# Performance work log

Hardware: AMD Instinct MI355X
Metric: run time of the kernel (lower is better)

The kernel has to match this reference:

```python
import jax, jax.numpy as jnp
import numpy as np

N_NODES = 50000
N_EDGES = 800000
DIM = 512
N_CLASSES = 1000


def _xavier(key, shape):
    fan_in, fan_out = shape[0], shape[1]
    lim = float(np.sqrt(6.0 / (fan_in + fan_out)))
    return jax.random.uniform(key, shape, jnp.float32, -lim, lim)


def setup_inputs() -> dict:
    key = jax.random.key(0)
    ks = jax.random.split(key, 12)
    nodes = jax.random.normal(ks[0], (N_NODES, DIM), jnp.float32)
    edges = jax.random.randint(ks[1], (2, N_EDGES), 0, N_NODES, jnp.int64)
    labelmatrix = jax.random.normal(ks[2], (N_CLASSES, 128), jnp.float32)
    return {
        "nodes": nodes,
        "edges": edges,
        "labelmatrix": labelmatrix,
        "W1": _xavier(ks[3], (DIM, 256)), "b1": jnp.zeros((256,), jnp.float32),
        "W2": _xavier(ks[4], (256, 192)), "b2": jnp.zeros((192,), jnp.float32),
        "W3": _xavier(ks[5], (192, 128)), "b3": jnp.zeros((128,), jnp.float32),
        "fc1_w": _xavier(ks[6], (128, 128)), "fc1_b": jnp.zeros((128,), jnp.float32),
        "fc2_w": _xavier(ks[7], (128, 128)), "fc2_b": jnp.zeros((128,), jnp.float32),
    }


def _gcn_conv(x, W, b, src, dst, n):
    # PyG GCNConv: add self-loops, symmetric normalization, then aggregate.
    xw = x @ W                                        # [N, out]
    ones = jnp.ones(src.shape[0], x.dtype)
    deg = jax.ops.segment_sum(ones, dst, num_segments=n) + 1.0  # +1 self-loop
    dinv = jax.lax.rsqrt(deg)                         # deg^{-1/2}
    coef = dinv[src] * dinv[dst]                      # [E]
    agg = jax.ops.segment_sum(xw[src] * coef[:, None], dst, num_segments=n)
    agg = agg + xw * (dinv * dinv)[:, None]           # self-loop contribution
    return agg + b


def reference(nodes, edges, labelmatrix, W1, b1, W2, b2, W3, b3,
              fc1_w, fc1_b, fc2_w, fc2_b):
    src, dst = edges[0], edges[1]
    n = nodes.shape[0]
    # _GraphConv: three stacked GCNConv layers, no inter-layer activation
    x = _gcn_conv(nodes, W1, b1, src, dst, n)
    x = _gcn_conv(x, W2, b2, src, dst, n)
    x = _gcn_conv(x, W3, b3, src, dst, n)             # [N, 128]
    # _GraphLinear (eval mode: dropout is identity)
    h = jax.nn.relu(x @ fc1_w + fc1_b)
    h = h @ fc2_w + fc2_b                             # [N, 128]
    preds = h @ labelmatrix.T                         # dot-product similarity [N, C]
    return preds
```

## Files before the change

### kernel.cpp

```cpp
#include <hip/hip_runtime.h>

typedef unsigned short u16;
typedef __bf16 bf16x8 __attribute__((ext_vector_type(8)));
typedef float f32x4 __attribute__((ext_vector_type(4)));

__device__ __forceinline__ u16 f2bf(float f) {
    unsigned int u = __float_as_uint(f);
    unsigned int r = (u + 0x7FFFu + ((u >> 16) & 1u)) >> 16;
    return (u16)r;
}
__device__ __forceinline__ float bf_lo(unsigned int u) { return __uint_as_float(u << 16); }
__device__ __forceinline__ float bf_hi(unsigned int u) { return __uint_as_float(u & 0xFFFF0000u); }

#define GLOAD_LDS(gp, lp) \
    __builtin_amdgcn_global_load_lds( \
        (const __attribute__((address_space(1))) unsigned int*)(gp), \
        (__attribute__((address_space(3))) unsigned int*)(lp), 16, 0, 0)


__global__ void hist_k(const int* __restrict__ dst, int* __restrict__ deg, int nE) {
    int e = blockIdx.x * 256 + threadIdx.x;
    if (e < nE) atomicAdd(&deg[dst[e]], 1);
}

__global__ void scan_block_k(const int* __restrict__ deg, int* __restrict__ scanned,
                             int* __restrict__ bsums, int n) {
    __shared__ int s[1024];
    int i = blockIdx.x * 1024 + threadIdx.x;
    int v = (i < n) ? deg[i] : 0;
    s[threadIdx.x] = v;
    __syncthreads();
    for (int off = 1; off < 1024; off <<= 1) {
        int t = (threadIdx.x >= off) ? s[threadIdx.x - off] : 0;
        __syncthreads();
        s[threadIdx.x] += t;
        __syncthreads();
    }
    if (i < n) scanned[i] = s[threadIdx.x];
    if (threadIdx.x == 1023) bsums[blockIdx.x] = s[1023];
}

__global__ void scan_sums_k(int* __restrict__ bsums, int nb) {
    int l = threadIdx.x & 63;
    int v = (l < nb) ? bsums[l] : 0;
    int orig = v;
    for (int off = 1; off < 64; off <<= 1) {
        int t = __shfl_up(v, off);
        if (l >= off) v += t;
    }
    if (l < nb) bsums[l] = v - orig;
}

__global__ void scan_final_dinv_k(const int* __restrict__ scanned, const int* __restrict__ deg,
                                  const int* __restrict__ bsums, int* __restrict__ rowptr,
                                  int* __restrict__ wptr, float* __restrict__ dinv,
                                  int n, int nE) {
    int i = blockIdx.x * 256 + threadIdx.x;
    if (i < n) {
        int rp = scanned[i] - deg[i] + bsums[i >> 10];
        rowptr[i] = rp;
        wptr[i] = rp;
        dinv[i] = rsqrtf((float)deg[i] + 1.0f);
    }
    if (i == 0) rowptr[n] = nE;
}

__global__ void csr_fill_k(const int* __restrict__ src, const int* __restrict__ dst,
                           int* __restrict__ wptr, const float* __restrict__ dinv,
                           int* __restrict__ eidx, float* __restrict__ ecoef, int nE) {
    int e = blockIdx.x * 256 + threadIdx.x;
    if (e >= nE) return;
    int d = dst[e], s = src[e];
    int p = atomicAdd(&wptr[d], 1);
    eidx[p] = s;
    ecoef[p] = dinv[s] * dinv[d];
}

__global__ void uv1_k(const int* __restrict__ rowptr, const float* __restrict__ ecoef,
                      const float* __restrict__ dinv, float* __restrict__ u1, int n) {
    int i = blockIdx.x * 256 + threadIdx.x;
    if (i >= n) return;
    float s = dinv[i] * dinv[i];
    int b = rowptr[i], e = rowptr[i + 1];
    for (int k = b; k < e; ++k) s += ecoef[k];
    u1[i] = s;
}

__global__ void uv2_k(const int* __restrict__ rowptr, const int* __restrict__ eidx,
                      const float* __restrict__ ecoef, const float* __restrict__ dinv,
                      const float* __restrict__ u1, float* __restrict__ u2, int n) {
    int i = blockIdx.x * 256 + threadIdx.x;
    if (i >= n) return;
    float s = dinv[i] * dinv[i] * u1[i];
    int b = rowptr[i], e = rowptr[i + 1];
    for (int k = b; k < e; ++k) s += ecoef[k] * u1[eidx[k]];
    u2[i] = s;
}


__global__ __launch_bounds__(192) void ck1_k(const float* __restrict__ W1,
                                             const float* __restrict__ W2,
                                             float* __restrict__ T1) {
    __shared__ float row[256];
    int i = blockIdx.x;
    for (int t = threadIdx.x; t < 256; t += 192) row[t] = W1[i * 256 + t];
    __syncthreads();
    int j = threadIdx.x;
    float s = 0.f;
    for (int k = 0; k < 256; ++k) s = fmaf(row[k], W2[k * 192 + j], s);
    T1[i * 192 + j] = s;
}

__global__ __launch_bounds__(256) void prep2_k(
    const float* __restrict__ T1, const float* __restrict__ W3, u16* __restrict__ Wp,
    const float* __restrict__ b1, const float* __restrict__ W2, const float* __restrict__ b2,
    float* __restrict__ c1, float* __restrict__ c2,
    const float* __restrict__ fc1_w, u16* __restrict__ Bfc1) {
    __shared__ float sbuf[192];
    const int b = blockIdx.x, tid = threadIdx.x;
    if (b < 512) {
        if (tid < 192) sbuf[tid] = T1[b * 192 + tid];
        __syncthreads();
        if (tid < 128) {
            float s = 0.f;
            for (int m = 0; m < 192; ++m) s = fmaf(sbuf[m], W3[m * 128 + tid], s);
            Wp[(size_t)tid * 512 + b] = f2bf(s);
        }
    } else if (b == 512) {
        if (tid < 192) {
            float s = 0.f;
            for (int k = 0; k < 256; ++k) s = fmaf(b1[k], W2[k * 192 + tid], s);
            sbuf[tid] = s;
        }
        __syncthreads();
        if (tid < 128) {
            float a = 0.f, bb = 0.f;
            for (int m = 0; m < 192; ++m) {
                a  = fmaf(sbuf[m], W3[m * 128 + tid], a);
                bb = fmaf(b2[m],   W3[m * 128 + tid], bb);
            }
            c1[tid] = a; c2[tid] = bb;
        }
    } else {
        int idx = (b - 513) * 256 + tid;
        if (idx < 128 * 128) {
            int nn = idx >> 7, k = idx & 127;
            Bfc1[idx] = f2bf(fc1_w[k * 128 + nn]);
        }
    }
}

__global__ __launch_bounds__(128) void fuse_fc2_k(
    const float* __restrict__ fc2_w, const float* __restrict__ fc2_b,
    const float* __restrict__ labelm, u16* __restrict__ Wc, float* __restrict__ bc) {
    __shared__ float w[128 * 129];
    __shared__ float lm[128];
    __shared__ float red[2];
    const int tid = threadIdx.x;
    for (int t = tid; t < 128 * 128; t += 128)
        w[(t >> 7) * 129 + (t & 127)] = fc2_w[t];
    __syncthreads();
    for (int cc = 0; cc < 8; ++cc) {
        int c = blockIdx.x * 8 + cc;
        lm[tid] = (c < 1000) ? labelm[(size_t)c * 128 + tid] : 0.f;
        __syncthreads();
        float sum = 0.f;
        const float* wr = &w[tid * 129];
        for (int j = 0; j < 128; ++j) sum = fmaf(wr[j], lm[j], sum);
        Wc[(size_t)c * 128 + tid] = f2bf(sum);
        float p = fc2_b[tid] * lm[tid];
        for (int off = 32; off > 0; off >>= 1) p += __shfl_down(p, off);
        if ((tid & 63) == 0) red[tid >> 6] = p;
        __syncthreads();
        if (tid == 0) bc[c] = red[0] + red[1];
        __syncthreads();
    }
}


template <bool CASTA, bool OUTF32, bool BIAS, bool RELU>
__global__ __launch_bounds__(256) void gemm_mfma(
    const void* __restrict__ Ap, const u16* __restrict__ Bt,
    const float* __restrict__ bias, void* __restrict__ Cout,
    int K, int Nout, int ldc, int Mout, int lgny, int Arows) {
    __shared__ __align__(16) u16 As[128 * 64];
    __shared__ __align__(16) u16 Bs[128 * 64];
    const int tid  = threadIdx.x;
    const int lane = tid & 63;
    const int w    = tid >> 6;
    const int wm   = w >> 1, wn = w & 1;

    const int nwg = gridDim.x, orig = blockIdx.x;
    const int q = nwg >> 3, r = nwg & 7;
    const int xcd = orig & 7, off = orig >> 3;
    const int tile = (xcd < r ? xcd * (q + 1) : r * (q + 1) + (xcd - r) * q) + off;
    const int ny = 1 << lgny;
    const int tx = tile >> lgny, ty = tile & (ny - 1);
    const size_t bm = (size_t)tx * 128;
    const size_t bn = (size_t)ty * 128;

    const int l7 = lane & 7;
    const int l3 = lane >> 3;
    const int kcs = l7 ^ l3;

    f32x4 acc[4][4] = {};

    for (int k0 = 0; k0 < K; k0 += 64) {
        if constexpr (CASTA) {
            const float* Af = (const float*)Ap;
            const int row = tid >> 1;
            const int half = tid & 1;
            const size_t grow = bm + row;
            const bool valid = grow < (size_t)Arows;
            const float4* g4 = (const float4*)(Af + grow * K + k0 + half * 32);
            float4 f[8];
#pragma unroll
            for (int j = 0; j < 8; ++j)
                f[j] = valid ? g4[j] : make_float4(0.f, 0.f, 0.f, 0.f);
#pragma unroll
            for (int j = 0; j < 4; ++j) {
                int kc = (half * 4 + j) ^ (row & 7);
                uint4 o;
                o.x = (unsigned)f2bf(f[2 * j].x)     | ((unsigned)f2bf(f[2 * j].y) << 16);
                o.y = (unsigned)f2bf(f[2 * j].z)     | ((unsigned)f2bf(f[2 * j].w) << 16);
                o.z = (unsigned)f2bf(f[2 * j + 1].x) | ((unsigned)f2bf(f[2 * j + 1].y) << 16);
                o.w = (unsigned)f2bf(f[2 * j + 1].z) | ((unsigned)f2bf(f[2 * j + 1].w) << 16);
                *(uint4*)((char*)As + row * 128 + kc * 16) = o;
            }
#pragma unroll
            for (int it = 0; it < 4; ++it) {
                const int r0 = w * 32 + it * 8;
                const u16* gB = Bt + ((size_t)(bn + r0 + l3) * K + k0) + kcs * 8;
                GLOAD_LDS(gB, Bs + r0 * 64);
            }
        } else {
            const u16* A = (const u16*)Ap;
#pragma unroll
            for (int it = 0; it < 4; ++it) {
                const int r0 = w * 32 + it * 8;
                const u16* gA = A + ((size_t)(bm + r0 + l3) * K + k0) + kcs * 8;
                GLOAD_LDS(gA, As + r0 * 64);
                const u16* gB = Bt + ((size_t)(bn + r0 + l3) * K + k0) + kcs * 8;
                GLOAD_LDS(gB, Bs + r0 * 64);
            }
        }
        __syncthreads();

#pragma unroll
        for (int ks = 0; ks < 2; ++ks) {
            bf16x8 av[4], bv[4];
#pragma unroll
            for (int i = 0; i < 4; ++i) {
                int row = wm * 64 + i * 16 + (lane & 15);
                int kc = (ks * 4 + (lane >> 4)) ^ (lane & 7);
                av[i] = *(const bf16x8*)((const char*)As + row * 128 + kc * 16);
            }
#pragma unroll
            for (int j = 0; j < 4; ++j) {
                int nn = wn * 64 + j * 16 + (lane & 15);
                int kc = (ks * 4 + (lane >> 4)) ^ (lane & 7);
                bv[j] = *(const bf16x8*)((const char*)Bs + nn * 128 + kc * 16);
            }
#pragma unroll
            for (int i = 0; i < 4; ++i)
#pragma unroll
                for (int j = 0; j < 4; ++j)
                    acc[i][j] = __builtin_amdgcn_mfma_f32_16x16x32_bf16(av[i], bv[j], acc[i][j], 0, 0, 0);
        }
        __syncthreads();
    }

    const int ccol  = lane & 15;
    const int crow4 = (lane >> 4) * 4;
#pragma unroll
    for (int i = 0; i < 4; ++i) {
#pragma unroll
        for (int j = 0; j < 4; ++j) {
#pragma unroll
            for (int r2 = 0; r2 < 4; ++r2) {
                size_t gr = bm + wm * 64 + i * 16 + crow4 + r2;
                size_t gc = bn + wn * 64 + j * 16 + ccol;
                if (gr < (size_t)Mout && gc < (size_t)Nout) {
                    float v = acc[i][j][r2];
                    if constexpr (BIAS) v += bias[gc];
                    if constexpr (RELU) v = fmaxf(v, 0.f);
                    if constexpr (OUTF32) ((float*)Cout)[gr * ldc + gc] = v;
                    else                  ((u16*)Cout)[gr * ldc + gc] = f2bf(v);
                }
            }
        }
    }
}


template <bool FINAL>
__global__ __launch_bounds__(256) void agg128_k(
    const u16* __restrict__ xw, const int* __restrict__ rowptr,
    const int* __restrict__ eidx, const float* __restrict__ ecoef,
    const float* __restrict__ dinv, u16* __restrict__ out,
    const float* __restrict__ u1v, const float* __restrict__ u2v,
    const float* __restrict__ c1, const float* __restrict__ c2,
    const float* __restrict__ b3, int n) {
    const int tid = threadIdx.x;
    const int sub = tid >> 4;
    const int fl  = tid & 15;
    int node = blockIdx.x * 16 + sub;
    if (node >= n) return;

    const uint4* xv = (const uint4*)xw;
    float di = dinv[node];
    float s = di * di;
    uint4 a = xv[(size_t)node * 16 + fl];
    float acc[8];
    acc[0] = s * bf_lo(a.x); acc[1] = s * bf_hi(a.x);
    acc[2] = s * bf_lo(a.y); acc[3] = s * bf_hi(a.y);
    acc[4] = s * bf_lo(a.z); acc[5] = s * bf_hi(a.z);
    acc[6] = s * bf_lo(a.w); acc[7] = s * bf_hi(a.w);

    const int beg = rowptr[node], end = rowptr[node + 1];
    int e = beg;
    for (; e + 7 < end; e += 8) {
        int sn[8]; float cf[8]; uint4 v[8];
#pragma unroll
        for (int q = 0; q < 8; ++q) { sn[q] = eidx[e + q]; cf[q] = ecoef[e + q]; }
#pragma unroll
        for (int q = 0; q < 8; ++q) v[q] = xv[(size_t)sn[q] * 16 + fl];
#pragma unroll
        for (int q = 0; q < 8; ++q) {
            acc[0] = fmaf(cf[q], bf_lo(v[q].x), acc[0]); acc[1] = fmaf(cf[q], bf_hi(v[q].x), acc[1]);
            acc[2] = fmaf(cf[q], bf_lo(v[q].y), acc[2]); acc[3] = fmaf(cf[q], bf_hi(v[q].y), acc[3]);
            acc[4] = fmaf(cf[q], bf_lo(v[q].z), acc[4]); acc[5] = fmaf(cf[q], bf_hi(v[q].z), acc[5]);
            acc[6] = fmaf(cf[q], bf_lo(v[q].w), acc[6]); acc[7] = fmaf(cf[q], bf_hi(v[q].w), acc[7]);
        }
    }
    for (; e < end; ++e) {
        int sn = eidx[e];
        float c = ecoef[e];
        uint4 v = xv[(size_t)sn * 16 + fl];
        acc[0] = fmaf(c, bf_lo(v.x), acc[0]); acc[1] = fmaf(c, bf_hi(v.x), acc[1]);
        acc[2] = fmaf(c, bf_lo(v.y), acc[2]); acc[3] = fmaf(c, bf_hi(v.y), acc[3]);
        acc[4] = fmaf(c, bf_lo(v.z), acc[4]); acc[5] = fmaf(c, bf_hi(v.z), acc[5]);
        acc[6] = fmaf(c, bf_lo(v.w), acc[6]); acc[7] = fmaf(c, bf_hi(v.w), acc[7]);
    }

    if constexpr (FINAL) {
        float uu1 = u1v[node], uu2 = u2v[node];
        float4 c1a = ((const float4*)c1)[fl * 2], c1b = ((const float4*)c1)[fl * 2 + 1];
        float4 c2a = ((const float4*)c2)[fl * 2], c2b = ((const float4*)c2)[fl * 2 + 1];
        float4 b3a = ((const float4*)b3)[fl * 2], b3b = ((const float4*)b3)[fl * 2 + 1];
        acc[0] += uu2 * c1a.x + uu1 * c2a.x + b3a.x;
        acc[1] += uu2 * c1a.y + uu1 * c2a.y + b3a.y;
        acc[2] += uu2 * c1a.z + uu1 * c2a.z + b3a.z;
        acc[3] += uu2 * c1a.w + uu1 * c2a.w + b3a.w;
        acc[4] += uu2 * c1b.x + uu1 * c2b.x + b3b.x;
        acc[5] += uu2 * c1b.y + uu1 * c2b.y + b3b.y;
        acc[6] += uu2 * c1b.z + uu1 * c2b.z + b3b.z;
        acc[7] += uu2 * c1b.w + uu1 * c2b.w + b3b.w;
    }

    uint4 o;
    o.x = (unsigned)f2bf(acc[0]) | ((unsigned)f2bf(acc[1]) << 16);
    o.y = (unsigned)f2bf(acc[2]) | ((unsigned)f2bf(acc[3]) << 16);
    o.z = (unsigned)f2bf(acc[4]) | ((unsigned)f2bf(acc[5]) << 16);
    o.w = (unsigned)f2bf(acc[6]) | ((unsigned)f2bf(acc[7]) << 16);
    ((uint4*)out)[(size_t)node * 16 + fl] = o;
}


extern "C" void kernel_launch(void* const* d_in, const int* in_sizes, int n_in,
                              void* d_out, int out_size, void* d_ws, size_t ws_size,
                              hipStream_t stream) {
    const float* nodes  = (const float*)d_in[0];
    const int*   edges  = (const int*)d_in[1];
    const float* labelm = (const float*)d_in[2];
    const float* W1 = (const float*)d_in[3];
    const float* b1 = (const float*)d_in[4];
    const float* W2 = (const float*)d_in[5];
    const float* b2 = (const float*)d_in[6];
    const float* W3 = (const float*)d_in[7];
    const float* b3 = (const float*)d_in[8];
    const float* fc1_w = (const float*)d_in[9];
    const float* fc1_b = (const float*)d_in[10];
    const float* fc2_w = (const float*)d_in[11];
    const float* fc2_b = (const float*)d_in[12];
    float* out = (float*)d_out;

    const int DIM = 512, N3 = 128, NC = 1000;
    const int n  = in_sizes[0] / DIM;
    const int nE = in_sizes[1] / 2;
    const int Mpad = 50048;
    const int* src = edges;
    const int* dst = edges + nE;

    u16* Y = (u16*)((char*)d_out + 67108864);
    u16* Z = (u16*)((char*)d_out + 100663296);

    char* ws = (char*)d_ws;
    u16*   Q      = (u16*)(ws);
    u16*   Rb     = (u16*)(ws + 12812288);
    float* T1     = (float*)(ws + 25624576);
    u16*   Wp     = (u16*)(ws + 26017792);
    u16*   Bfc1   = (u16*)(ws + 26148864);
    u16*   Wc     = (u16*)(ws + 26181632);
    float* bc     = (float*)(ws + 26443776);
    float* c1     = (float*)(ws + 26447872);
    float* c2     = (float*)(ws + 26448384);
    float* u1     = (float*)(ws + 26448896);
    float* u2     = (float*)(ws + 26648896);
    int*   deg_i  = (int*)(ws + 26848896);
    float* dinv   = (float*)(ws + 27048896);
    int*   rowptr = (int*)(ws + 27248896);
    int*   wptr   = (int*)(ws + 27448960);
    int*   scanned= (int*)(ws + 27648960);
    int*   bsums  = (int*)(ws + 27848960);
    int*   eidx   = (int*)(ws + 27849216);
    float* ecoef  = (float*)(ws + 31049216);

    hipMemsetAsync(deg_i, 0, (size_t)n * 4, stream);
    hist_k<<<(nE + 255) / 256, 256, 0, stream>>>(dst, deg_i, nE);
    int nb = (n + 1023) / 1024;
    scan_block_k<<<nb, 1024, 0, stream>>>(deg_i, scanned, bsums, n);
    scan_sums_k<<<1, 64, 0, stream>>>(bsums, nb);
    scan_final_dinv_k<<<(n + 255) / 256, 256, 0, stream>>>(scanned, deg_i, bsums, rowptr, wptr, dinv, n, nE);
    csr_fill_k<<<(nE + 255) / 256, 256, 0, stream>>>(src, dst, wptr, dinv, eidx, ecoef, nE);
    uv1_k<<<(n + 255) / 256, 256, 0, stream>>>(rowptr, ecoef, dinv, u1, n);
    uv2_k<<<(n + 255) / 256, 256, 0, stream>>>(rowptr, eidx, ecoef, dinv, u1, u2, n);

    ck1_k<<<512, 192, 0, stream>>>(W1, W2, T1);
    prep2_k<<<577, 256, 0, stream>>>(T1, W3, Wp, b1, W2, b2, c1, c2, fc1_w, Bfc1);
    fuse_fc2_k<<<128, 128, 0, stream>>>(fc2_w, fc2_b, labelm, Wc, bc);

    const int gx = Mpad / 128;
    dim3 blk(256);
    const int gagg = (n + 15) / 16;

    gemm_mfma<true, false, false, false><<<gx, blk, 0, stream>>>(nodes, Wp, nullptr, Y, 512, N3, N3, Mpad, 0, n);
    agg128_k<false><<<gagg, blk, 0, stream>>>(Y, rowptr, eidx, ecoef, dinv, Z, nullptr, nullptr, nullptr, nullptr, nullptr, n);
    agg128_k<false><<<gagg, blk, 0, stream>>>(Z, rowptr, eidx, ecoef, dinv, Y, nullptr, nullptr, nullptr, nullptr, nullptr, n);
    agg128_k<true ><<<gagg, blk, 0, stream>>>(Y, rowptr, eidx, ecoef, dinv, Rb, u1, u2, c1, c2, b3, n);
    gemm_mfma<false, false, true, true><<<gx, blk, 0, stream>>>(Rb, Bfc1, fc1_b, Q, 128, N3, N3, Mpad, 0, Mpad);
    gemm_mfma<false, true, true, false><<<gx * 8, blk, 0, stream>>>(Q, Wc, bc, out, 128, NC, NC, n, 3, Mpad);
}
```

Measured before the change: 396.4 us.

## Fold u1/u2 sums into aggregation passes and merge weight prep kernels

Removes the separate uv1/uv2 kernels by computing the coefficient sums inside the first and third aggregation passes. The scan_sums launch is dropped by having each thread sum the block totals directly, and ck1/prep2/fuse_fc2 are merged into one prep kernel. The aim is fewer launches and less time spent in small serial kernels. In exchange the aggregation kernels carry extra per-edge work (a gather of u1 in the third pass), and the merged prep kernel uses large shared memory for every block, which may lower its occupancy.

```diff
diff --git a/kernel.cpp b/kernel.cpp
--- a/kernel.cpp
+++ b/kernel.cpp
@@ -40,24 +40,16 @@
     if (threadIdx.x == 1023) bsums[blockIdx.x] = s[1023];
 }
 
-__global__ void scan_sums_k(int* __restrict__ bsums, int nb) {
-    int l = threadIdx.x & 63;
-    int v = (l < nb) ? bsums[l] : 0;
-    int orig = v;
-    for (int off = 1; off < 64; off <<= 1) {
-        int t = __shfl_up(v, off);
-        if (l >= off) v += t;
-    }
-    if (l < nb) bsums[l] = v - orig;
-}
-
 __global__ void scan_final_dinv_k(const int* __restrict__ scanned, const int* __restrict__ deg,
                                   const int* __restrict__ bsums, int* __restrict__ rowptr,
                                   int* __restrict__ wptr, float* __restrict__ dinv,
                                   int n, int nE) {
     int i = blockIdx.x * 256 + threadIdx.x;
     if (i < n) {
-        int rp = scanned[i] - deg[i] + bsums[i >> 10];
+        int pre = 0;
+        int nbi = i >> 10;
+        for (int j = 0; j < nbi; ++j) pre += bsums[j];
+        int rp = scanned[i] - deg[i] + pre;
         rowptr[i] = rp;
         wptr[i] = rp;
         dinv[i] = rsqrtf((float)deg[i] + 1.0f);
@@ -76,104 +68,79 @@
     ecoef[p] = dinv[s] * dinv[d];
 }
 
-__global__ void uv1_k(const int* __restrict__ rowptr, const float* __restrict__ ecoef,
-                      const float* __restrict__ dinv, float* __restrict__ u1, int n) {
-    int i = blockIdx.x * 256 + threadIdx.x;
-    if (i >= n) return;
-    float s = dinv[i] * dinv[i];
-    int b = rowptr[i], e = rowptr[i + 1];
-    for (int k = b; k < e; ++k) s += ecoef[k];
-    u1[i] = s;
-}
-
-__global__ void uv2_k(const int* __restrict__ rowptr, const int* __restrict__ eidx,
-                      const float* __restrict__ ecoef, const float* __restrict__ dinv,
-                      const float* __restrict__ u1, float* __restrict__ u2, int n) {
-    int i = blockIdx.x * 256 + threadIdx.x;
-    if (i >= n) return;
-    float s = dinv[i] * dinv[i] * u1[i];
-    int b = rowptr[i], e = rowptr[i + 1];
-    for (int k = b; k < e; ++k) s += ecoef[k] * u1[eidx[k]];
-    u2[i] = s;
-}
-
-
-__global__ __launch_bounds__(192) void ck1_k(const float* __restrict__ W1,
-                                             const float* __restrict__ W2,
-                                             float* __restrict__ T1) {
-    __shared__ float row[256];
-    int i = blockIdx.x;
-    for (int t = threadIdx.x; t < 256; t += 192) row[t] = W1[i * 256 + t];
-    __syncthreads();
-    int j = threadIdx.x;
-    float s = 0.f;
-    for (int k = 0; k < 256; ++k) s = fmaf(row[k], W2[k * 192 + j], s);
-    T1[i * 192 + j] = s;
-}
-
-__global__ __launch_bounds__(256) void prep2_k(
-    const float* __restrict__ T1, const float* __restrict__ W3, u16* __restrict__ Wp,
-    const float* __restrict__ b1, const float* __restrict__ W2, const float* __restrict__ b2,
-    float* __restrict__ c1, float* __restrict__ c2,
-    const float* __restrict__ fc1_w, u16* __restrict__ Bfc1) {
-    __shared__ float sbuf[192];
+
+__global__ __launch_bounds__(256) void prep_all_k(
+    const float* __restrict__ W1, const float* __restrict__ W2, const float* __restrict__ W3,
+    const float* __restrict__ b1, const float* __restrict__ b2,
+    const float* __restrict__ fc1_w, const float* __restrict__ fc2_w,
+    const float* __restrict__ fc2_b, const float* __restrict__ labelm,
+    u16* __restrict__ Wp, float* __restrict__ c1, float* __restrict__ c2,
+    u16* __restrict__ Bfc1, u16* __restrict__ Wc, float* __restrict__ bc) {
+    __shared__ float lds[16706];
     const int b = blockIdx.x, tid = threadIdx.x;
     if (b < 512) {
-        if (tid < 192) sbuf[tid] = T1[b * 192 + tid];
+        float* row = lds;
+        float* t1r = lds + 256;
+        row[tid] = (tid < 256) ? W1[b * 256 + tid] : 0.f;
+        __syncthreads();
+        if (tid < 192) {
+            float s = 0.f;
+            for (int k = 0; k < 256; ++k) s = fmaf(row[k], W2[k * 192 + tid], s);
+            t1r[tid] = s;
+        }
         __syncthreads();
         if (tid < 128) {
             float s = 0.f;
-            for (int m = 0; m < 192; ++m) s = fmaf(sbuf[m], W3[m * 128 + tid], s);
+            for (int m = 0; m < 192; ++m) s = fmaf(t1r[m], W3[m * 128 + tid], s);
             Wp[(size_t)tid * 512 + b] = f2bf(s);
         }
     } else if (b == 512) {
+        float* t1b = lds;
         if (tid < 192) {
             float s = 0.f;
             for (int k = 0; k < 256; ++k) s = fmaf(b1[k], W2[k * 192 + tid], s);
-            sbuf[tid] = s;
+            t1b[tid] = s;
         }
         __syncthreads();
         if (tid < 128) {
             float a = 0.f, bb = 0.f;
             for (int m = 0; m < 192; ++m) {
-                a  = fmaf(sbuf[m], W3[m * 128 + tid], a);
-                bb = fmaf(b2[m],   W3[m * 128 + tid], bb);
+                a  = fmaf(t1b[m], W3[m * 128 + tid], a);
+                bb = fmaf(b2[m],  W3[m * 128 + tid], bb);
             }
             c1[tid] = a; c2[tid] = bb;
         }
-    } else {
+    } else if (b < 577) {
         int idx = (b - 513) * 256 + tid;
         if (idx < 128 * 128) {
             int nn = idx >> 7, k = idx & 127;
             Bfc1[idx] = f2bf(fc1_w[k * 128 + nn]);
         }
-    }
-}
-
-__global__ __launch_bounds__(128) void fuse_fc2_k(
-    const float* __restrict__ fc2_w, const float* __restrict__ fc2_b,
-    const float* __restrict__ labelm, u16* __restrict__ Wc, float* __restrict__ bc) {
-    __shared__ float w[128 * 129];
-    __shared__ float lm[128];
-    __shared__ float red[2];
-    const int tid = threadIdx.x;
-    for (int t = tid; t < 128 * 128; t += 128)
-        w[(t >> 7) * 129 + (t & 127)] = fc2_w[t];
-    __syncthreads();
-    for (int cc = 0; cc < 8; ++cc) {
-        int c = blockIdx.x * 8 + cc;
-        lm[tid] = (c < 1000) ? labelm[(size_t)c * 128 + tid] : 0.f;
-        __syncthreads();
-        float sum = 0.f;
-        const float* wr = &w[tid * 129];
-        for (int j = 0; j < 128; ++j) sum = fmaf(wr[j], lm[j], sum);
-        Wc[(size_t)c * 128 + tid] = f2bf(sum);
-        float p = fc2_b[tid] * lm[tid];
-        for (int off = 32; off > 0; off >>= 1) p += __shfl_down(p, off);
-        if ((tid & 63) == 0) red[tid >> 6] = p;
-        __syncthreads();
-        if (tid == 0) bc[c] = red[0] + red[1];
-        __syncthreads();
+    } else {
+        const int cb = b - 577;
+        float* w  = lds;
+        float* lm = lds + 16512;
+        float* red = lds + 16640;
+        for (int t = tid; t < 128 * 128; t += 256)
+            w[(t >> 7) * 129 + (t & 127)] = fc2_w[t];
+        __syncthreads();
+        for (int cc = 0; cc < 8; ++cc) {
+            int c = cb * 8 + cc;
+            if (tid < 128) lm[tid] = (c < 1000) ? labelm[(size_t)c * 128 + tid] : 0.f;
+            __syncthreads();
+            if (tid < 128) {
+                float sum = 0.f;
+                const float* wr = &w[tid * 129];
+                for (int j = 0; j < 128; ++j) sum = fmaf(wr[j], lm[j], sum);
+                Wc[(size_t)c * 128 + tid] = f2bf(sum);
+                float p = fc2_b[tid] * lm[tid];
+                for (int off = 32; off > 0; off >>= 1) p += __shfl_down(p, off);
+                if ((tid & 63) == 0) red[tid >> 6] = p;
+            }
+            __syncthreads();
+            if (tid == 0) bc[c] = red[0] + red[1];
+            __syncthreads();
+        }
     }
 }
 
@@ -293,14 +260,13 @@
 }
 
 
-template <bool FINAL>
+template <int MODE>
 __global__ __launch_bounds__(256) void agg128_k(
     const u16* __restrict__ xw, const int* __restrict__ rowptr,
     const int* __restrict__ eidx, const float* __restrict__ ecoef,
     const float* __restrict__ dinv, u16* __restrict__ out,
-    const float* __restrict__ u1v, const float* __restrict__ u2v,
-    const float* __restrict__ c1, const float* __restrict__ c2,
-    const float* __restrict__ b3, int n) {
+    float* __restrict__ u1, const float* __restrict__ c1,
+    const float* __restrict__ c2, const float* __restrict__ b3, int n) {
     const int tid = threadIdx.x;
     const int sub = tid >> 4;
     const int fl  = tid & 15;
@@ -316,6 +282,7 @@
     acc[2] = s * bf_lo(a.y); acc[3] = s * bf_hi(a.y);
     acc[4] = s * bf_lo(a.z); acc[5] = s * bf_hi(a.z);
     acc[6] = s * bf_lo(a.w); acc[7] = s * bf_hi(a.w);
+    float usum = 0.f;
 
     const int beg = rowptr[node], end = rowptr[node + 1];
     int e = beg;
@@ -327,6 +294,8 @@
         for (int q = 0; q < 8; ++q) v[q] = xv[(size_t)sn[q] * 16 + fl];
 #pragma unroll
         for (int q = 0; q < 8; ++q) {
+            if constexpr (MODE == 0) usum += cf[q];
+            if constexpr (MODE == 2) usum = fmaf(cf[q], u1[sn[q]], usum);
             acc[0] = fmaf(cf[q], bf_lo(v[q].x), acc[0]); acc[1] = fmaf(cf[q], bf_hi(v[q].x), acc[1]);
             acc[2] = fmaf(cf[q], bf_lo(v[q].y), acc[2]); acc[3] = fmaf(cf[q], bf_hi(v[q].y), acc[3]);
             acc[4] = fmaf(cf[q], bf_lo(v[q].z), acc[4]); acc[5] = fmaf(cf[q], bf_hi(v[q].z), acc[5]);
@@ -337,25 +306,31 @@
         int sn = eidx[e];
         float c = ecoef[e];
         uint4 v = xv[(size_t)sn * 16 + fl];
+        if constexpr (MODE == 0) usum += c;
+        if constexpr (MODE == 2) usum = fmaf(c, u1[sn], usum);
         acc[0] = fmaf(c, bf_lo(v.x), acc[0]); acc[1] = fmaf(c, bf_hi(v.x), acc[1]);
         acc[2] = fmaf(c, bf_lo(v.y), acc[2]); acc[3] = fmaf(c, bf_hi(v.y), acc[3]);
         acc[4] = fmaf(c, bf_lo(v.z), acc[4]); acc[5] = fmaf(c, bf_hi(v.z), acc[5]);
         acc[6] = fmaf(c, bf_lo(v.w), acc[6]); acc[7] = fmaf(c, bf_hi(v.w), acc[7]);
     }
 
-    if constexpr (FINAL) {
-        float uu1 = u1v[node], uu2 = u2v[node];
+    if constexpr (MODE == 0) {
+        if (fl == 0) u1[node] = s + usum;
+    }
+    if constexpr (MODE == 2) {
+        float u1n = u1[node];
+        float u2n = s * u1n + usum;
         float4 c1a = ((const float4*)c1)[fl * 2], c1b = ((const float4*)c1)[fl * 2 + 1];
         float4 c2a = ((const float4*)c2)[fl * 2], c2b = ((const float4*)c2)[fl * 2 + 1];
         float4 b3a = ((const float4*)b3)[fl * 2], b3b = ((const float4*)b3)[fl * 2 + 1];
-        acc[0] += uu2 * c1a.x + uu1 * c2a.x + b3a.x;
-        acc[1] += uu2 * c1a.y + uu1 * c2a.y + b3a.y;
-        acc[2] += uu2 * c1a.z + uu1 * c2a.z + b3a.z;
-        acc[3] += uu2 * c1a.w + uu1 * c2a.w + b3a.w;
-        acc[4] += uu2 * c1b.x + uu1 * c2b.x + b3b.x;
-        acc[5] += uu2 * c1b.y + uu1 * c2b.y + b3b.y;
-        acc[6] += uu2 * c1b.z + uu1 * c2b.z + b3b.z;
-        acc[7] += uu2 * c1b.w + uu1 * c2b.w + b3b.w;
+        acc[0] += u2n * c1a.x + u1n * c2a.x + b3a.x;
+        acc[1] += u2n * c1a.y + u1n * c2a.y + b3a.y;
+        acc[2] += u2n * c1a.z + u1n * c2a.z + b3a.z;
+        acc[3] += u2n * c1a.w + u1n * c2a.w + b3a.w;
+        acc[4] += u2n * c1b.x + u1n * c2b.x + b3b.x;
+        acc[5] += u2n * c1b.y + u1n * c2b.y + b3b.y;
+        acc[6] += u2n * c1b.z + u1n * c2b.z + b3b.z;
+        acc[7] += u2n * c1b.w + u1n * c2b.w + b3b.w;
     }
 
     uint4 o;
@@ -398,7 +373,6 @@
     char* ws = (char*)d_ws;
     u16*   Q      = (u16*)(ws);
     u16*   Rb     = (u16*)(ws + 12812288);
-    float* T1     = (float*)(ws + 25624576);
     u16*   Wp     = (u16*)(ws + 26017792);
     u16*   Bfc1   = (u16*)(ws + 26148864);
     u16*   Wc     = (u16*)(ws + 26181632);
@@ -406,7 +380,6 @@
     float* c1     = (float*)(ws + 26447872);
     float* c2     = (float*)(ws + 26448384);
     float* u1     = (float*)(ws + 26448896);
-    float* u2     = (float*)(ws + 26648896);
     int*   deg_i  = (int*)(ws + 26848896);
     float* dinv   = (float*)(ws + 27048896);
     int*   rowptr = (int*)(ws + 27248896);
@@ -420,24 +393,20 @@
     hist_k<<<(nE + 255) / 256, 256, 0, stream>>>(dst, deg_i, nE);
     int nb = (n + 1023) / 1024;
     scan_block_k<<<nb, 1024, 0, stream>>>(deg_i, scanned, bsums, n);
-    scan_sums_k<<<1, 64, 0, stream>>>(bsums, nb);
     scan_final_dinv_k<<<(n + 255) / 256, 256, 0, stream>>>(scanned, deg_i, bsums, rowptr, wptr, dinv, n, nE);
     csr_fill_k<<<(nE + 255) / 256, 256, 0, stream>>>(src, dst, wptr, dinv, eidx, ecoef, nE);
-    uv1_k<<<(n + 255) / 256, 256, 0, stream>>>(rowptr, ecoef, dinv, u1, n);
-    uv2_k<<<(n + 255) / 256, 256, 0, stream>>>(rowptr, eidx, ecoef, dinv, u1, u2, n);
-
-    ck1_k<<<512, 192, 0, stream>>>(W1, W2, T1);
-    prep2_k<<<577, 256, 0, stream>>>(T1, W3, Wp, b1, W2, b2, c1, c2, fc1_w, Bfc1);
-    fuse_fc2_k<<<128, 128, 0, stream>>>(fc2_w, fc2_b, labelm, Wc, bc);
+
+    prep_all_k<<<705, 256, 0, stream>>>(W1, W2, W3, b1, b2, fc1_w, fc2_w, fc2_b, labelm,
+                                        Wp, c1, c2, Bfc1, Wc, bc);
 
     const int gx = Mpad / 128;
     dim3 blk(256);
     const int gagg = (n + 15) / 16;
 
     gemm_mfma<true, false, false, false><<<gx, blk, 0, stream>>>(nodes, Wp, nullptr, Y, 512, N3, N3, Mpad, 0, n);
-    agg128_k<false><<<gagg, blk, 0, stream>>>(Y, rowptr, eidx, ecoef, dinv, Z, nullptr, nullptr, nullptr, nullptr, nullptr, n);
-    agg128_k<false><<<gagg, blk, 0, stream>>>(Z, rowptr, eidx, ecoef, dinv, Y, nullptr, nullptr, nullptr, nullptr, nullptr, n);
-    agg128_k<true ><<<gagg, blk, 0, stream>>>(Y, rowptr, eidx, ecoef, dinv, Rb, u1, u2, c1, c2, b3, n);
+    agg128_k<0><<<gagg, blk, 0, stream>>>(Y, rowptr, eidx, ecoef, dinv, Z, u1, nullptr, nullptr, nullptr, n);
+    agg128_k<1><<<gagg, blk, 0, stream>>>(Z, rowptr, eidx, ecoef, dinv, Y, nullptr, nullptr, nullptr, nullptr, n);
+    agg128_k<2><<<gagg, blk, 0, stream>>>(Y, rowptr, eidx, ecoef, dinv, Rb, u1, c1, c2, b3, n);
     gemm_mfma<false, false, true, true><<<gx, blk, 0, stream>>>(Rb, Bfc1, fc1_b, Q, 128, N3, N3, Mpad, 0, Mpad);
     gemm_mfma<false, true, true, false><<<gx * 8, blk, 0, stream>>>(Q, Wc, bc, out, 128, NC, NC, n, 3, Mpad);
 }
```

Result: faster. 371.0 us (-6.4%).
